# Performance work log

Hardware: AMD Instinct MI355X
Metric: run time of the kernel (lower is better)

The kernel has to match this reference:

```python
import jax, jax.numpy as jnp
import numpy as np

CLAMP = 10000.0
EPS = 1e-8
NUM_HEADS = 4


def _sanitize(t):
    t = jnp.nan_to_num(t, nan=0.0, posinf=CLAMP, neginf=-CLAMP)
    return jnp.clip(t, -CLAMP, CLAMP)


def _rmsnorm(t, w):
    # Matches the torch module: L2-norm based RMS, eps added OUTSIDE the sqrt.
    t = _sanitize(t)
    d = t.shape[-1]
    rms = jnp.linalg.norm(t, axis=-1, keepdims=True) * (1.0 / np.sqrt(float(d)))
    return w * (t / (rms + EPS))


def setup_inputs() -> dict:
    key = jax.random.key(0)
    ks = jax.random.split(key, 7)
    N, C, S = 100000, 1024, 18
    x = jax.random.normal(ks[0], (N, C), dtype=jnp.float32)
    seeds = jax.random.normal(ks[1], (S, C), dtype=jnp.float32) / np.sqrt(float(C))
    w_nq = jnp.ones((C,), dtype=jnp.float32)
    w_nkv = jnp.ones((C,), dtype=jnp.float32)
    # nn.MultiheadAttention params (xavier-ish scale)
    in_proj_w = jax.random.normal(ks[2], (3 * C, C), dtype=jnp.float32) * (1.0 / np.sqrt(float(C)))
    in_proj_b = jnp.zeros((3 * C,), dtype=jnp.float32)
    out_proj_w = jax.random.normal(ks[3], (C, C), dtype=jnp.float32) * (1.0 / np.sqrt(float(C)))
    out_proj_b = jnp.zeros((C,), dtype=jnp.float32)
    return {"x": x, "seeds": seeds, "w_nq": w_nq, "w_nkv": w_nkv,
            "in_proj_w": in_proj_w, "in_proj_b": in_proj_b,
            "out_proj_w": out_proj_w, "out_proj_b": out_proj_b}


def reference(x, seeds, w_nq, w_nkv, in_proj_w, in_proj_b, out_proj_w, out_proj_b):
    x = _sanitize(x)
    N, C = x.shape
    S = seeds.shape[0]
    H = NUM_HEADS
    Dh = C // H

    q = _rmsnorm(seeds, w_nq)      # (S, C)
    kv = _rmsnorm(x, w_nkv)        # (N, C) -- same tensor feeds both k and v

    Wq, Wk, Wv = in_proj_w[:C], in_proj_w[C:2 * C], in_proj_w[2 * C:]
    bq, bk, bv = in_proj_b[:C], in_proj_b[C:2 * C], in_proj_b[2 * C:]

    qp = (q @ Wq.T + bq).reshape(S, H, Dh) * (1.0 / np.sqrt(float(Dh)))
    kp = (kv @ Wk.T + bk).reshape(N, H, Dh)
    vp = (kv @ Wv.T + bv).reshape(N, H, Dh)

    # (H, S, N) scores -- S=18 << N, skinny attention
    scores = jnp.einsum('shd,nhd->hsn', qp, kp)
    attn = jax.nn.softmax(scores, axis=-1)
    o = jnp.einsum('hsn,nhd->shd', attn, vp).reshape(S, C)

    y = o @ out_proj_w.T + out_proj_b   # (S, C)
    ctx = _sanitize(y.mean(axis=0))     # (C,)
    return ctx
```

## Files before the change

kernel.cpp:

```cpp
#include <hip/hip_runtime.h>
#include <math.h>

#define NTOK 100000
#define C 1024
#define SN 18
#define H 4
#define DH 256
#define HSN 72
#define CLAMPV 10000.0f
#define EPSV 1e-8f

using short8 = __attribute__((ext_vector_type(8))) short;
using f32x4  = __attribute__((ext_vector_type(4))) float;

__device__ __forceinline__ float sanitize_f(float v) {
    if (isnan(v)) return 0.0f;
    return fminf(CLAMPV, fmaxf(-CLAMPV, v));
}
__device__ __forceinline__ unsigned short f2bf(float f) {
    unsigned int u = __float_as_uint(f);
    u = (u + 0x7FFFu + ((u >> 16) & 1u)) >> 16;
    return (unsigned short)u;
}
__device__ __forceinline__ float waveSum(float v) {
    #pragma unroll
    for (int o = 32; o > 0; o >>= 1) v += __shfl_down(v, o, 64);
    return v;
}
__device__ __forceinline__ float waveMax(float v) {
    #pragma unroll
    for (int o = 32; o > 0; o >>= 1) v = fmaxf(v, __shfl_down(v, o, 64));
    return v;
}

__global__ void k_qnorm(const float* __restrict__ seeds, const float* __restrict__ w_nq,
                        float* __restrict__ q) {
    int row = blockIdx.x, tid = threadIdx.x;
    const float* src = seeds + (size_t)row * C;
    float ss = 0.f;
    for (int c = tid; c < C; c += 256) { float v = sanitize_f(src[c]); ss += v * v; }
    __shared__ float red[4]; __shared__ float sSc;
    float w = waveSum(ss);
    if ((tid & 63) == 0) red[tid >> 6] = w;
    __syncthreads();
    if (tid == 0) {
        float t = red[0] + red[1] + red[2] + red[3];
        float rms = sqrtf(t / (float)C);
        sSc = 1.0f / (rms + EPSV);
    }
    __syncthreads();
    float sc = sSc;
    for (int c = tid; c < C; c += 256) q[(size_t)row * C + c] = w_nq[c] * sanitize_f(src[c]) * sc;
}

__global__ void k_qp(const float* __restrict__ q, const float* __restrict__ Wq,
                     const float* __restrict__ bq, float* __restrict__ qp) {
    int tid = threadIdx.x, wid = tid >> 6, lane = tid & 63;
    int out = blockIdx.x * 4 + wid;
    int s = out >> 10, j = out & 1023;
    const float* qrow = q + (size_t)s * C;
    const float* wrow = Wq + (size_t)j * C;
    float acc = 0.f;
    #pragma unroll
    for (int k = 0; k < 16; ++k) { int c = lane + 64 * k; acc = fmaf(qrow[c], wrow[c], acc); }
    acc = waveSum(acc);
    if (lane == 0) qp[out] = (acc + bq[j]) * 0.0625f;
}

__global__ void k_U(const float* __restrict__ qp, const float* __restrict__ in_proj_w,
                    const float* __restrict__ w_nkv, unsigned short* __restrict__ Ub) {
    int b = blockIdx.x, tid = threadIdx.x;
    int row = b >> 2, ct = b & 3;
    int c = ct * 256 + tid;
    __shared__ float qps[DH];
    if (row < HSN) {
        int h = row / SN, s = row % SN;
        qps[tid] = qp[(size_t)s * C + h * DH + tid];
        __syncthreads();
        const float* Wk = in_proj_w + (size_t)C * C;
        float acc = 0.f;
        #pragma unroll 4
        for (int d = 0; d < DH; ++d) acc = fmaf(qps[d], Wk[(size_t)(h * DH + d) * C + c], acc);
        Ub[(size_t)row * C + c] = f2bf(acc * w_nkv[c]);
    } else {
        Ub[(size_t)row * C + c] = 0;
    }
}

__global__ void k_bsc(const float* __restrict__ qp, const float* __restrict__ in_proj_b,
                      float* __restrict__ bsc) {
    int tid = threadIdx.x, wid = tid >> 6, lane = tid & 63;
    int hs = blockIdx.x * 4 + wid;
    int h = hs / SN, s = hs % SN;
    const float* bk = in_proj_b + C;
    float acc = 0.f;
    #pragma unroll
    for (int k = 0; k < 4; ++k) {
        int d = lane + 64 * k;
        acc = fmaf(qp[(size_t)s * C + h * DH + d], bk[h * DH + d], acc);
    }
    acc = waveSum(acc);
    if (lane == 0) bsc[hs] = acc;
}

__global__ __launch_bounds__(256, 3) void k_passA(const float* __restrict__ x,
    const unsigned short* __restrict__ Ub, const float* __restrict__ bsc,
    float* __restrict__ scaleG, float* __restrict__ scoresG) {
    __shared__ unsigned short xbL[8192];
    __shared__ unsigned short UbL[5120];
    __shared__ float bscLds[HSN];
    __shared__ float scaleLds[128];
    int tid = threadIdx.x;
    int n0 = blockIdx.x * 128;
    if (tid < HSN) bscLds[tid] = bsc[tid];
    int lane = tid & 63, wv = tid >> 6;
    int q = lane >> 4, mn = lane & 15;
    f32x4 acc[5][2];
    #pragma unroll
    for (int mt = 0; mt < 5; ++mt)
        #pragma unroll
        for (int nt = 0; nt < 2; ++nt) acc[mt][nt] = (f32x4){0.f, 0.f, 0.f, 0.f};
    float ss[8];
    #pragma unroll
    for (int i = 0; i < 8; ++i) ss[i] = 0.f;

    for (int kt = 0; kt < 16; ++kt) {
        __syncthreads();
        #pragma unroll
        for (int i = 0; i < 8; ++i) {
            int f = tid + 256 * i;
            int tok = f >> 4, cq = f & 15;
            int n = n0 + tok;
            float4 v = make_float4(0.f, 0.f, 0.f, 0.f);
            if (n < NTOK) v = *(const float4*)(x + (size_t)n * C + kt * 64 + 4 * cq);
            v.x = sanitize_f(v.x); v.y = sanitize_f(v.y);
            v.z = sanitize_f(v.z); v.w = sanitize_f(v.w);
            ss[i] += v.x * v.x + v.y * v.y + v.z * v.z + v.w * v.w;
            unsigned int lo = (unsigned int)f2bf(v.x) | ((unsigned int)f2bf(v.y) << 16);
            unsigned int hi = (unsigned int)f2bf(v.z) | ((unsigned int)f2bf(v.w) << 16);
            int ks = cq >> 3, c32 = (cq & 7) * 4;
            *(uint2*)&xbL[ks * 4096 + tok * 32 + c32] = make_uint2(lo, hi);
        }
        #pragma unroll
        for (int u = 0; u < 5; ++u) {
            int idx = tid + 256 * u;
            int row = idx >> 4, cq = idx & 15;
            int ks = cq >> 3, c32 = (cq & 7) * 4;
            uint2 w4 = *(const uint2*)(Ub + (size_t)row * C + kt * 64 + 4 * cq);
            *(uint2*)&UbL[ks * 2560 + row * 32 + c32] = w4;
        }
        __syncthreads();
        #pragma unroll
        for (int ks = 0; ks < 2; ++ks) {
            short8 a[5], b[2];
            #pragma unroll
            for (int mt = 0; mt < 5; ++mt)
                a[mt] = *(const short8*)&UbL[ks * 2560 + (mt * 16 + mn) * 32 + q * 8];
            #pragma unroll
            for (int nt = 0; nt < 2; ++nt)
                b[nt] = *(const short8*)&xbL[ks * 4096 + (wv * 32 + nt * 16 + mn) * 32 + q * 8];
            #pragma unroll
            for (int mt = 0; mt < 5; ++mt)
                #pragma unroll
                for (int nt = 0; nt < 2; ++nt)
                    acc[mt][nt] = __builtin_amdgcn_mfma_f32_16x16x32_bf16(a[mt], b[nt], acc[mt][nt], 0, 0, 0);
        }
    }
    __syncthreads();
    float* ssS = (float*)xbL;
    #pragma unroll
    for (int i = 0; i < 8; ++i) ssS[((tid >> 4) + 16 * i) * 17 + (tid & 15)] = ss[i];
    __syncthreads();
    if (tid < 128) {
        float t = 0.f;
        #pragma unroll
        for (int k = 0; k < 16; ++k) t += ssS[tid * 17 + k];
        float rms = sqrtf(t / (float)C);
        float sc = 1.0f / (rms + EPSV);
        scaleLds[tid] = sc;
        if (n0 + tid < NTOK) scaleG[n0 + tid] = sc;
    }
    __syncthreads();
    #pragma unroll
    for (int mt = 0; mt < 5; ++mt) {
        #pragma unroll
        for (int nt = 0; nt < 2; ++nt) {
            int tl = wv * 32 + nt * 16 + mn;
            int n = n0 + tl;
            #pragma unroll
            for (int r = 0; r < 4; ++r) {
                int hs = mt * 16 + q * 4 + r;
                if (hs < HSN && n < NTOK)
                    scoresG[(size_t)hs * NTOK + n] = acc[mt][nt][r] * scaleLds[tl] + bscLds[hs];
            }
        }
    }
}

__global__ void k_stats1(const float* __restrict__ scoresG, float* __restrict__ pm,
                         float* __restrict__ pd) {
    int ch = blockIdx.x, hs = blockIdx.y, tid = threadIdx.x;
    int nbeg = ch * 6250, nend = nbeg + 6250;
    if (nend > NTOK) nend = NTOK;
    const float* row = scoresG + (size_t)hs * NTOK;
    float m = -INFINITY;
    for (int n = nbeg + tid; n < nend; n += 256) m = fmaxf(m, row[n]);
    __shared__ float red[4]; __shared__ float sM;
    float w = waveMax(m);
    if ((tid & 63) == 0) red[tid >> 6] = w;
    __syncthreads();
    if (tid == 0) sM = fmaxf(fmaxf(red[0], red[1]), fmaxf(red[2], red[3]));
    __syncthreads();
    float mm = sM;
    float sum = 0.f;
    for (int n = nbeg + tid; n < nend; n += 256) sum += __expf(row[n] - mm);
    __syncthreads();
    float ws2 = waveSum(sum);
    if ((tid & 63) == 0) red[tid >> 6] = ws2;
    __syncthreads();
    if (tid == 0) { pm[hs * 16 + ch] = mm; pd[hs * 16 + ch] = red[0] + red[1] + red[2] + red[3]; }
}

__global__ void k_stats2(const float* __restrict__ pm, const float* __restrict__ pd,
                         float* __restrict__ mx, float* __restrict__ den) {
    int t = threadIdx.x;
    if (t >= HSN) return;
    float m = -INFINITY;
    #pragma unroll
    for (int i = 0; i < 16; ++i) m = fmaxf(m, pm[t * 16 + i]);
    float s = 0.f;
    #pragma unroll
    for (int i = 0; i < 16; ++i) s += pd[t * 16 + i] * __expf(pm[t * 16 + i] - m);
    mx[t] = m; den[t] = s;
}

__global__ __launch_bounds__(256, 3) void k_passB(const float* __restrict__ x,
    const float* __restrict__ scoresG, const float* __restrict__ mx,
    const float* __restrict__ den, const float* __restrict__ scaleG,
    float* __restrict__ Praw) {
    __shared__ unsigned short xbTL[8192];
    __shared__ unsigned short wTL[5120];
    __shared__ float mxL[80], idL[80], sL[64];
    int tid = threadIdx.x;
    int id = blockIdx.x;
    int r8 = id & 7, k8 = id >> 3;
    int cb = k8 & 7;
    int tch = r8 + 8 * (k8 >> 3);
    if (tch >= 98) return;
    int c0 = cb * 128;
    if (tid < 80) {
        if (tid < HSN) { mxL[tid] = mx[tid]; idL[tid] = 1.0f / den[tid]; }
        else { mxL[tid] = 0.f; idL[tid] = 0.f; }
    }
    int lane = tid & 63, wv = tid >> 6;
    int q = lane >> 4, mn = lane & 15;
    f32x4 acc[5][2];
    #pragma unroll
    for (int mt = 0; mt < 5; ++mt)
        #pragma unroll
        for (int nt = 0; nt < 2; ++nt) acc[mt][nt] = (f32x4){0.f, 0.f, 0.f, 0.f};

    for (int scn = 0; scn < 16; ++scn) {
        int n0 = tch * 1024 + scn * 64;
        __syncthreads();
        if (tid < 16) *(float4*)&sL[tid * 4] = *(const float4*)(scaleG + n0 + tid * 4);
        __syncthreads();
        #pragma unroll
        for (int u = 0; u < 5; ++u) {
            int idx = tid + 256 * u;
            int hs = idx >> 4, tq = idx & 15;
            int ks = tq >> 3, t32 = (tq & 7) * 4;
            int nbase = n0 + 4 * tq;
            unsigned int lo = 0, hi = 0;
            if (hs < HSN && nbase < NTOK) {
                float4 s4 = *(const float4*)(scoresG + (size_t)hs * NTOK + nbase);
                float mh = mxL[hs], ih = idL[hs];
                float w0 = __expf(s4.x - mh) * sL[4 * tq + 0] * ih;
                float w1 = __expf(s4.y - mh) * sL[4 * tq + 1] * ih;
                float w2 = __expf(s4.z - mh) * sL[4 * tq + 2] * ih;
                float w3 = __expf(s4.w - mh) * sL[4 * tq + 3] * ih;
                lo = (unsigned int)f2bf(w0) | ((unsigned int)f2bf(w1) << 16);
                hi = (unsigned int)f2bf(w2) | ((unsigned int)f2bf(w3) << 16);
            }
            *(uint2*)&wTL[ks * 2560 + hs * 32 + t32] = make_uint2(lo, hi);
        }
        #pragma unroll
        for (int g = 0; g < 4; ++g) {
            int half = tid >> 7;
            int cL = tid & 127;
            int tok0 = 32 * half + 8 * g;
            union { unsigned short u16[8]; short8 v; } pk;
            #pragma unroll
            for (int j = 0; j < 8; ++j) {
                int n = n0 + tok0 + j;
                float xv = 0.f;
                if (n < NTOK) xv = x[(size_t)n * C + c0 + cL];
                pk.u16[j] = f2bf(sanitize_f(xv));
            }
            *(short8*)&xbTL[half * 4096 + cL * 32 + 8 * g] = pk.v;
        }
        __syncthreads();
        #pragma unroll
        for (int ks = 0; ks < 2; ++ks) {
            short8 a[5], b[2];
            #pragma unroll
            for (int mt = 0; mt < 5; ++mt)
                a[mt] = *(const short8*)&wTL[ks * 2560 + (mt * 16 + mn) * 32 + q * 8];
            #pragma unroll
            for (int nt = 0; nt < 2; ++nt)
                b[nt] = *(const short8*)&xbTL[ks * 4096 + (wv * 32 + nt * 16 + mn) * 32 + q * 8];
            #pragma unroll
            for (int mt = 0; mt < 5; ++mt)
                #pragma unroll
                for (int nt = 0; nt < 2; ++nt)
                    acc[mt][nt] = __builtin_amdgcn_mfma_f32_16x16x32_bf16(a[mt], b[nt], acc[mt][nt], 0, 0, 0);
        }
    }
    #pragma unroll
    for (int mt = 0; mt < 5; ++mt) {
        #pragma unroll
        for (int r = 0; r < 4; ++r) {
            int hs = mt * 16 + q * 4 + r;
            if (hs < HSN) {
                #pragma unroll
                for (int nt = 0; nt < 2; ++nt) {
                    int cc = c0 + wv * 32 + nt * 16 + mn;
                    atomicAdd(Praw + (size_t)hs * C + cc, acc[mt][nt][r]);
                }
            }
        }
    }
}

__global__ void k_o(const float* __restrict__ Praw, const float* __restrict__ in_proj_w,
                    const float* __restrict__ in_proj_b, const float* __restrict__ w_nkv,
                    float* __restrict__ o) {
    int tid = threadIdx.x, wid = tid >> 6, lane = tid & 63;
    int out = blockIdx.x * 4 + wid;
    int s = out >> 10, hd = out & 1023;
    int h = hd >> 8;
    int hs = h * SN + s;
    const float* Wv = in_proj_w + (size_t)2 * C * C + (size_t)hd * C;
    const float* P = Praw + (size_t)hs * C;
    float acc = 0.f;
    #pragma unroll
    for (int k = 0; k < 16; ++k) { int c = lane + 64 * k; acc = fmaf(Wv[c], w_nkv[c] * P[c], acc); }
    acc = waveSum(acc);
    if (lane == 0) o[(size_t)s * C + hd] = acc + in_proj_b[2 * C + hd];
}

__global__ void k_obar(const float* __restrict__ o, float* __restrict__ obar) {
    int c = blockIdx.x * 256 + threadIdx.x;
    float acc = 0.f;
    #pragma unroll
    for (int s = 0; s < SN; ++s) acc += o[(size_t)s * C + c];
    obar[c] = acc * (1.0f / (float)SN);
}

__global__ void k_out(const float* __restrict__ obar, const float* __restrict__ Wout,
                      const float* __restrict__ bout, float* __restrict__ outp) {
    int tid = threadIdx.x, wid = tid >> 6, lane = tid & 63;
    int j = blockIdx.x * 4 + wid;
    float acc = 0.f;
    #pragma unroll
    for (int k = 0; k < 16; ++k) { int c = lane + 64 * k; acc = fmaf(obar[c], Wout[(size_t)j * C + c], acc); }
    acc = waveSum(acc);
    if (lane == 0) outp[j] = sanitize_f(acc + bout[j]);
}

extern "C" void kernel_launch(void* const* d_in, const int* in_sizes, int n_in,
                              void* d_out, int out_size, void* d_ws, size_t ws_size,
                              hipStream_t stream) {
    (void)in_sizes; (void)n_in; (void)out_size; (void)ws_size;
    const float* x         = (const float*)d_in[0];
    const float* seeds     = (const float*)d_in[1];
    const float* w_nq      = (const float*)d_in[2];
    const float* w_nkv     = (const float*)d_in[3];
    const float* in_proj_w = (const float*)d_in[4];
    const float* in_proj_b = (const float*)d_in[5];
    const float* out_proj_w = (const float*)d_in[6];
    const float* out_proj_b = (const float*)d_in[7];
    float* outp = (float*)d_out;

    float* ws     = (float*)d_ws;
    float* q      = ws;
    float* qp     = ws + 18432;
    unsigned short* Ub = (unsigned short*)(ws + 36864);
    float* bsc    = ws + 110592;
    float* mxA    = ws + 110720;
    float* den    = ws + 110848;
    float* scale  = ws + 110976;
    float* pm     = ws + 211328;
    float* pd     = ws + 212480;
    float* scores = ws + 213632;
    float* Praw   = ws + 7413632;
    float* o      = ws + 7487360;
    float* obar   = ws + 7505792;

    k_qnorm<<<SN, 256, 0, stream>>>(seeds, w_nq, q);
    k_qp<<<4608, 256, 0, stream>>>(q, in_proj_w, in_proj_b, qp);
    k_U<<<320, 256, 0, stream>>>(qp, in_proj_w, w_nkv, Ub);
    k_bsc<<<SN, 256, 0, stream>>>(qp, in_proj_b, bsc);
    k_passA<<<782, 256, 0, stream>>>(x, Ub, bsc, scale, scores);
    k_stats1<<<dim3(16, HSN), 256, 0, stream>>>(scores, pm, pd);
    k_stats2<<<1, 128, 0, stream>>>(pm, pd, mxA, den);
    hipMemsetAsync(Praw, 0, (size_t)HSN * C * sizeof(float), stream);
    k_passB<<<832, 256, 0, stream>>>(x, scores, mxA, den, scale, Praw);
    k_o<<<4608, 256, 0, stream>>>(Praw, in_proj_w, in_proj_b, w_nkv, o);
    k_obar<<<4, 256, 0, stream>>>(o, obar);
    k_out<<<256, 256, 0, stream>>>(obar, out_proj_w, out_proj_b, outp);
}
```

Measured before the change: 855.4 us.

## Cache bf16 x from pass A and precompute softmax weights for pass B

Pass A can now also write the sanitized bf16 copy of x to workspace, so pass B reads 2-byte values instead of re-reading fp32 x and converting it. This path is enabled only when the workspace is large enough. A new kernel computes the normalized softmax weights once in bf16, folding in the old stats2 step, so pass B no longer recomputes exponentials redundantly per channel block. The bsc computation is folded into k_U and stats1 now uses float4 loads. In exchange, pass A writes about 200MB of extra data, and whether the xb path runs depends on the harness workspace size.

```diff
diff --git a/kernel.cpp b/kernel.cpp
--- a/kernel.cpp
+++ b/kernel.cpp
@@ -68,15 +68,24 @@
 }
 
 __global__ void k_U(const float* __restrict__ qp, const float* __restrict__ in_proj_w,
-                    const float* __restrict__ w_nkv, unsigned short* __restrict__ Ub) {
+                    const float* __restrict__ in_proj_b, const float* __restrict__ w_nkv,
+                    unsigned short* __restrict__ Ub, float* __restrict__ bsc) {
     int b = blockIdx.x, tid = threadIdx.x;
     int row = b >> 2, ct = b & 3;
     int c = ct * 256 + tid;
     __shared__ float qps[DH];
+    __shared__ float red2[4];
     if (row < HSN) {
         int h = row / SN, s = row % SN;
         qps[tid] = qp[(size_t)s * C + h * DH + tid];
         __syncthreads();
+        if (ct == 0) {
+            float pb = qps[tid] * in_proj_b[C + h * DH + tid];
+            float wsum = waveSum(pb);
+            if ((tid & 63) == 0) red2[tid >> 6] = wsum;
+            __syncthreads();
+            if (tid == 0) bsc[row] = red2[0] + red2[1] + red2[2] + red2[3];
+        }
         const float* Wk = in_proj_w + (size_t)C * C;
         float acc = 0.f;
         #pragma unroll 4
@@ -87,25 +96,10 @@
     }
 }
 
-__global__ void k_bsc(const float* __restrict__ qp, const float* __restrict__ in_proj_b,
-                      float* __restrict__ bsc) {
-    int tid = threadIdx.x, wid = tid >> 6, lane = tid & 63;
-    int hs = blockIdx.x * 4 + wid;
-    int h = hs / SN, s = hs % SN;
-    const float* bk = in_proj_b + C;
-    float acc = 0.f;
-    #pragma unroll
-    for (int k = 0; k < 4; ++k) {
-        int d = lane + 64 * k;
-        acc = fmaf(qp[(size_t)s * C + h * DH + d], bk[h * DH + d], acc);
-    }
-    acc = waveSum(acc);
-    if (lane == 0) bsc[hs] = acc;
-}
-
 __global__ __launch_bounds__(256, 3) void k_passA(const float* __restrict__ x,
     const unsigned short* __restrict__ Ub, const float* __restrict__ bsc,
-    float* __restrict__ scaleG, float* __restrict__ scoresG) {
+    float* __restrict__ scaleG, float* __restrict__ scoresG,
+    unsigned short* __restrict__ xbG, int writeXb) {
     __shared__ unsigned short xbL[8192];
     __shared__ unsigned short UbL[5120];
     __shared__ float bscLds[HSN];
@@ -138,6 +132,8 @@
             ss[i] += v.x * v.x + v.y * v.y + v.z * v.z + v.w * v.w;
             unsigned int lo = (unsigned int)f2bf(v.x) | ((unsigned int)f2bf(v.y) << 16);
             unsigned int hi = (unsigned int)f2bf(v.z) | ((unsigned int)f2bf(v.w) << 16);
+            if (writeXb && n < NTOK)
+                *(uint2*)&xbG[(size_t)n * C + kt * 64 + 4 * cq] = make_uint2(lo, hi);
             int ks = cq >> 3, c32 = (cq & 7) * 4;
             *(uint2*)&xbL[ks * 4096 + tok * 32 + c32] = make_uint2(lo, hi);
         }
@@ -200,11 +196,14 @@
 __global__ void k_stats1(const float* __restrict__ scoresG, float* __restrict__ pm,
                          float* __restrict__ pd) {
     int ch = blockIdx.x, hs = blockIdx.y, tid = threadIdx.x;
-    int nbeg = ch * 6250, nend = nbeg + 6250;
+    int nbeg = ch * 6272, nend = nbeg + 6272;
     if (nend > NTOK) nend = NTOK;
     const float* row = scoresG + (size_t)hs * NTOK;
     float m = -INFINITY;
-    for (int n = nbeg + tid; n < nend; n += 256) m = fmaxf(m, row[n]);
+    for (int n = nbeg + 4 * tid; n < nend; n += 1024) {
+        float4 v = *(const float4*)(row + n);
+        m = fmaxf(fmaxf(m, fmaxf(v.x, v.y)), fmaxf(v.z, v.w));
+    }
     __shared__ float red[4]; __shared__ float sM;
     float w = waveMax(m);
     if ((tid & 63) == 0) red[tid >> 6] = w;
@@ -213,7 +212,10 @@
     __syncthreads();
     float mm = sM;
     float sum = 0.f;
-    for (int n = nbeg + tid; n < nend; n += 256) sum += __expf(row[n] - mm);
+    for (int n = nbeg + 4 * tid; n < nend; n += 1024) {
+        float4 v = *(const float4*)(row + n);
+        sum += __expf(v.x - mm) + __expf(v.y - mm) + __expf(v.z - mm) + __expf(v.w - mm);
+    }
     __syncthreads();
     float ws2 = waveSum(sum);
     if ((tid & 63) == 0) red[tid >> 6] = ws2;
@@ -221,26 +223,39 @@
     if (tid == 0) { pm[hs * 16 + ch] = mm; pd[hs * 16 + ch] = red[0] + red[1] + red[2] + red[3]; }
 }
 
-__global__ void k_stats2(const float* __restrict__ pm, const float* __restrict__ pd,
-                         float* __restrict__ mx, float* __restrict__ den) {
-    int t = threadIdx.x;
-    if (t >= HSN) return;
-    float m = -INFINITY;
-    #pragma unroll
-    for (int i = 0; i < 16; ++i) m = fmaxf(m, pm[t * 16 + i]);
-    float s = 0.f;
-    #pragma unroll
-    for (int i = 0; i < 16; ++i) s += pd[t * 16 + i] * __expf(pm[t * 16 + i] - m);
-    mx[t] = m; den[t] = s;
-}
-
+__global__ void k_w(const float* __restrict__ scoresG, const float* __restrict__ pm,
+                    const float* __restrict__ pd, const float* __restrict__ scaleG,
+                    unsigned short* __restrict__ wb) {
+    int hs = blockIdx.y;
+    __shared__ float sM, sI;
+    if (threadIdx.x == 0) {
+        float m = -INFINITY;
+        #pragma unroll
+        for (int i = 0; i < 16; ++i) m = fmaxf(m, pm[hs * 16 + i]);
+        float s = 0.f;
+        #pragma unroll
+        for (int i = 0; i < 16; ++i) s += pd[hs * 16 + i] * __expf(pm[hs * 16 + i] - m);
+        sM = m; sI = 1.0f / s;
+    }
+    __syncthreads();
+    int n = (blockIdx.x * 256 + threadIdx.x) * 4;
+    if (n >= NTOK) return;
+    float mh = sM, ih = sI;
+    float4 s4 = *(const float4*)(scoresG + (size_t)hs * NTOK + n);
+    float4 c4 = *(const float4*)(scaleG + n);
+    unsigned int lo = (unsigned int)f2bf(__expf(s4.x - mh) * c4.x * ih)
+                    | ((unsigned int)f2bf(__expf(s4.y - mh) * c4.y * ih) << 16);
+    unsigned int hi = (unsigned int)f2bf(__expf(s4.z - mh) * c4.z * ih)
+                    | ((unsigned int)f2bf(__expf(s4.w - mh) * c4.w * ih) << 16);
+    *(uint2*)&wb[(size_t)hs * NTOK + n] = make_uint2(lo, hi);
+}
+
+template<int USE_XB>
 __global__ __launch_bounds__(256, 3) void k_passB(const float* __restrict__ x,
-    const float* __restrict__ scoresG, const float* __restrict__ mx,
-    const float* __restrict__ den, const float* __restrict__ scaleG,
+    const unsigned short* __restrict__ xb, const unsigned short* __restrict__ wb,
     float* __restrict__ Praw) {
     __shared__ unsigned short xbTL[8192];
     __shared__ unsigned short wTL[5120];
-    __shared__ float mxL[80], idL[80], sL[64];
     int tid = threadIdx.x;
     int id = blockIdx.x;
     int r8 = id & 7, k8 = id >> 3;
@@ -248,10 +263,6 @@
     int tch = r8 + 8 * (k8 >> 3);
     if (tch >= 98) return;
     int c0 = cb * 128;
-    if (tid < 80) {
-        if (tid < HSN) { mxL[tid] = mx[tid]; idL[tid] = 1.0f / den[tid]; }
-        else { mxL[tid] = 0.f; idL[tid] = 0.f; }
-    }
     int lane = tid & 63, wv = tid >> 6;
     int q = lane >> 4, mn = lane & 15;
     f32x4 acc[5][2];
@@ -263,26 +274,16 @@
     for (int scn = 0; scn < 16; ++scn) {
         int n0 = tch * 1024 + scn * 64;
         __syncthreads();
-        if (tid < 16) *(float4*)&sL[tid * 4] = *(const float4*)(scaleG + n0 + tid * 4);
-        __syncthreads();
         #pragma unroll
         for (int u = 0; u < 5; ++u) {
             int idx = tid + 256 * u;
-            int hs = idx >> 4, tq = idx & 15;
+            int hsr = idx >> 4, tq = idx & 15;
             int ks = tq >> 3, t32 = (tq & 7) * 4;
             int nbase = n0 + 4 * tq;
-            unsigned int lo = 0, hi = 0;
-            if (hs < HSN && nbase < NTOK) {
-                float4 s4 = *(const float4*)(scoresG + (size_t)hs * NTOK + nbase);
-                float mh = mxL[hs], ih = idL[hs];
-                float w0 = __expf(s4.x - mh) * sL[4 * tq + 0] * ih;
-                float w1 = __expf(s4.y - mh) * sL[4 * tq + 1] * ih;
-                float w2 = __expf(s4.z - mh) * sL[4 * tq + 2] * ih;
-                float w3 = __expf(s4.w - mh) * sL[4 * tq + 3] * ih;
-                lo = (unsigned int)f2bf(w0) | ((unsigned int)f2bf(w1) << 16);
-                hi = (unsigned int)f2bf(w2) | ((unsigned int)f2bf(w3) << 16);
-            }
-            *(uint2*)&wTL[ks * 2560 + hs * 32 + t32] = make_uint2(lo, hi);
+            uint2 w4 = make_uint2(0u, 0u);
+            if (hsr < HSN && nbase < NTOK)
+                w4 = *(const uint2*)&wb[(size_t)hsr * NTOK + nbase];
+            *(uint2*)&wTL[ks * 2560 + hsr * 32 + t32] = w4;
         }
         #pragma unroll
         for (int g = 0; g < 4; ++g) {
@@ -293,9 +294,13 @@
             #pragma unroll
             for (int j = 0; j < 8; ++j) {
                 int n = n0 + tok0 + j;
-                float xv = 0.f;
-                if (n < NTOK) xv = x[(size_t)n * C + c0 + cL];
-                pk.u16[j] = f2bf(sanitize_f(xv));
+                if (USE_XB) {
+                    pk.u16[j] = (n < NTOK) ? xb[(size_t)n * C + c0 + cL] : (unsigned short)0;
+                } else {
+                    float xv = 0.f;
+                    if (n < NTOK) xv = x[(size_t)n * C + c0 + cL];
+                    pk.u16[j] = f2bf(sanitize_f(xv));
+                }
             }
             *(short8*)&xbTL[half * 4096 + cL * 32 + 8 * g] = pk.v;
         }
@@ -371,7 +376,7 @@
 extern "C" void kernel_launch(void* const* d_in, const int* in_sizes, int n_in,
                               void* d_out, int out_size, void* d_ws, size_t ws_size,
                               hipStream_t stream) {
-    (void)in_sizes; (void)n_in; (void)out_size; (void)ws_size;
+    (void)in_sizes; (void)n_in; (void)out_size;
     const float* x         = (const float*)d_in[0];
     const float* seeds     = (const float*)d_in[1];
     const float* w_nq      = (const float*)d_in[2];
@@ -387,8 +392,6 @@
     float* qp     = ws + 18432;
     unsigned short* Ub = (unsigned short*)(ws + 36864);
     float* bsc    = ws + 110592;
-    float* mxA    = ws + 110720;
-    float* den    = ws + 110848;
     float* scale  = ws + 110976;
     float* pm     = ws + 211328;
     float* pd     = ws + 212480;
@@ -396,16 +399,21 @@
     float* Praw   = ws + 7413632;
     float* o      = ws + 7487360;
     float* obar   = ws + 7505792;
+    unsigned short* wb = (unsigned short*)(ws + 7506816);
+    unsigned short* xb = (unsigned short*)(ws + 11110400);
+    int useXb = (ws_size >= (size_t)249241600ull) ? 1 : 0;
 
     k_qnorm<<<SN, 256, 0, stream>>>(seeds, w_nq, q);
     k_qp<<<4608, 256, 0, stream>>>(q, in_proj_w, in_proj_b, qp);
-    k_U<<<320, 256, 0, stream>>>(qp, in_proj_w, w_nkv, Ub);
-    k_bsc<<<SN, 256, 0, stream>>>(qp, in_proj_b, bsc);
-    k_passA<<<782, 256, 0, stream>>>(x, Ub, bsc, scale, scores);
+    k_U<<<320, 256, 0, stream>>>(qp, in_proj_w, in_proj_b, w_nkv, Ub, bsc);
+    k_passA<<<782, 256, 0, stream>>>(x, Ub, bsc, scale, scores, xb, useXb);
     k_stats1<<<dim3(16, HSN), 256, 0, stream>>>(scores, pm, pd);
-    k_stats2<<<1, 128, 0, stream>>>(pm, pd, mxA, den);
+    k_w<<<dim3(98, HSN), 256, 0, stream>>>(scores, pm, pd, scale, wb);
     hipMemsetAsync(Praw, 0, (size_t)HSN * C * sizeof(float), stream);
-    k_passB<<<832, 256, 0, stream>>>(x, scores, mxA, den, scale, Praw);
+    if (useXb)
+        k_passB<1><<<832, 256, 0, stream>>>(x, xb, wb, Praw);
+    else
+        k_passB<0><<<832, 256, 0, stream>>>(x, xb, wb, Praw);
     k_o<<<4608, 256, 0, stream>>>(Praw, in_proj_w, in_proj_b, w_nkv, o);
     k_obar<<<4, 256, 0, stream>>>(o, obar);
     k_out<<<256, 256, 0, stream>>>(obar, out_proj_w, out_proj_b, outp);
```

Result: slower. 886.4 us (+3.6%).
